# Performance work log

Measured on AMD Instinct MI355X. Metric: run time of the kernel, lower is better.

## Reference

```python
import jax, jax.numpy as jnp
from jax import lax
from jax.scipy.special import logsumexp
import numpy as np

N_NODES = 6144
N_EDGES = 98304
N_FEAT = 128
N_TPLT = 16
M_NODES = 10
N_CG = 5        # conditional-gradient (Frank-Wolfe) outer iterations
N_SINK = 50     # log-domain Sinkhorn iterations for the linearized OT subproblem


def setup_inputs() -> dict:
    key = jax.random.key(0)
    k1, k2, k3, k4 = jax.random.split(key, 4)
    x = jax.random.normal(k1, (N_NODES, N_FEAT), dtype=jnp.float32)
    edge_index = jax.random.randint(k2, (2, N_EDGES), 0, N_NODES, dtype=jnp.int64)
    # template_initialisation: uniform(0,1) adjacencies, symmetrized; normal features; zero q0/alpha0
    t_raw = jax.random.uniform(k3, (N_TPLT, M_NODES, M_NODES), dtype=jnp.float32)
    templates = 0.5 * (t_raw + jnp.transpose(t_raw, (0, 2, 1)))
    templates_features = jax.random.normal(k4, (N_TPLT, M_NODES, N_FEAT), dtype=jnp.float32)
    q0 = jnp.zeros((N_TPLT, M_NODES), dtype=jnp.float32)
    alpha0 = jnp.zeros((1,), dtype=jnp.float32)
    return {"x": x, "edge_index": edge_index, "templates": templates,
            "templates_features": templates_features, "q0": q0, "alpha0": alpha0}


def _sinkhorn_log(G, logp, logq, reg):
    """Log-domain Sinkhorn solving min <G,T> + reg*H(T) over U(p,q)."""
    K = -G / reg                         # [n, m]
    f0 = jnp.zeros_like(logp)

    def body(f, _):
        g = logq - logsumexp(K + f[:, None], axis=0)
        f = logp - logsumexp(K + g[None, :], axis=1)
        return f, None

    f, _ = lax.scan(body, f0, None, length=N_SINK)
    g = logq - logsumexp(K + f[:, None], axis=0)
    return jnp.exp(f[:, None] + K + g[None, :])


def _fgw2(M, C1, C2, p, q, alpha):
    """Fused Gromov-Wasserstein distance (square loss) via conditional gradient.
    M: [n,m] feature cost, C1: [n,n] graph structure, C2: [m,m] template structure."""
    # init_matrix (square loss): constC = f1(C1) p 1^T + 1 q^T f2(C2)^T
    constC = (C1 ** 2 @ p)[:, None] + (C2 ** 2 @ q)[None, :]   # [n, m]
    logp, logq = jnp.log(p), jnp.log(q)
    T0 = p[:, None] * q[None, :]

    def step(T, _):
        C1TC2 = C1 @ T @ C2                                   # [n, m] (dominant cost)
        grad = (1.0 - alpha) * M + alpha * 2.0 * (constC - 2.0 * C1TC2)
        reg = lax.stop_gradient(0.05 * jnp.max(jnp.abs(grad)) + 1e-8)
        Tn = _sinkhorn_log(grad, logp, logq, reg)             # linearized OT subproblem
        dT = Tn - T
        # exact line search for the quadratic objective along dT
        C1dTC2 = C1 @ dT @ C2
        a = -2.0 * alpha * jnp.sum(C1dTC2 * dT)
        b = (1.0 - alpha) * jnp.sum(M * dT) + alpha * (jnp.sum(constC * dT) - 4.0 * jnp.sum(C1TC2 * dT))
        tau = jnp.where(a > 0.0,
                        jnp.clip(-b / (2.0 * a + 1e-16), 0.0, 1.0),
                        jnp.where(a + b < 0.0, 1.0, 0.0))
        return T + tau * dT, None

    T, _ = lax.scan(step, T0, None, length=N_CG)
    gw = jnp.sum((constC - 2.0 * (C1 @ T @ C2)) * T)
    wass = jnp.sum(M * T)
    return (1.0 - alpha) * wass + alpha * gw


def reference(x, edge_index, templates, templates_features, q0, alpha0):
    alpha = jax.nn.sigmoid(alpha0)[0]
    q = jax.nn.softmax(q0, axis=1)                            # [T, m] template node weights
    n = x.shape[0]
    # dense adjacency from edge list (symmetrized)
    A = jnp.zeros((n, n), dtype=x.dtype).at[edge_index[0], edge_index[1]].set(1.0)
    C1 = jnp.maximum(A, A.T)                                  # [n, n]
    p = jnp.full((n,), 1.0 / n, dtype=x.dtype)
    # squared euclidean feature cost per template: [T, n, m]
    M = (jnp.sum(x ** 2, axis=1)[None, :, None]
         + jnp.sum(templates_features ** 2, axis=-1)[:, None, :]
         - 2.0 * jnp.einsum('nf,tmf->tnm', x, templates_features))
    dists = jax.vmap(_fgw2, in_axes=(0, None, 0, None, 0, None))(M, C1, templates, p, q, alpha)
    return dists                                              # [n_templates]
```

## Files before the change

### kernel.cpp

```cpp
#include <hip/hip_runtime.h>
#include <hip/hip_cooperative_groups.h>

namespace cgx = cooperative_groups;

static constexpr int NN  = 6144;
static constexpr int NE  = 98304;
static constexpr int NF  = 128;
static constexpr int NT  = 16;
static constexpr int MN  = 10;
static constexpr int NCG = 5;
static constexpr int NSK = 50;
static constexpr int WPR = NN / 32;
static constexpr int TPB = 768;
static constexpr int NBLK = 256;
static constexpr int RPT = NN / TPB;
static constexpr int NW  = TPB / 64;

static_assert(TPB * RPT == NN, "row mapping");

static constexpr size_t OFF_M   = 0;
static constexpr size_t OFF_T4  = OFF_M  + (size_t)NT * NN * MN;
static constexpr size_t OFF_T1  = OFF_T4 + (size_t)NT * NN * 4;
static constexpr size_t OFF_C4  = OFF_T1 + (size_t)NT * NN;
static constexpr size_t OFF_C1  = OFF_C4 + (size_t)NT * NN * 4;
static constexpr size_t OFF_D4  = OFF_C1 + (size_t)NT * NN;
static constexpr size_t OFF_D1  = OFF_D4 + (size_t)NT * NN * 4;
static constexpr size_t OFF_RS  = OFF_D1 + (size_t)NT * NN;
static constexpr size_t OFF_DEG = OFF_RS + NN;
static constexpr size_t OFF_CI  = OFF_DEG + NN;
static constexpr size_t OFF_NNZ = OFF_CI + NE;

static constexpr int LDS_PL  = NN * 20;
static constexpr int LDS_SP  = TPB * 7 * 4;
static constexpr int LDS_DYN = LDS_PL + LDS_SP;

__device__ __forceinline__ unsigned f2bf(float f) {
    unsigned u = __float_as_uint(f);
    return (u + 0x7fffu + ((u >> 16) & 1u)) >> 16;
}
__device__ __forceinline__ unsigned packbf(float a, float b) { return f2bf(a) | (f2bf(b) << 16); }
__device__ __forceinline__ float bflo(unsigned w) { return __uint_as_float(w << 16); }
__device__ __forceinline__ float bfhi(unsigned w) { return __uint_as_float(w & 0xffff0000u); }

extern __shared__ char sMem[];

__global__ __launch_bounds__(TPB) void tfgw_kernel(
    const float* __restrict__ x, const void* __restrict__ eiv,
    const float* __restrict__ tpl, const float* __restrict__ tf,
    const float* __restrict__ q0, const float* __restrict__ a0,
    float* __restrict__ out, float* __restrict__ W)
{
    __shared__ float sC2[MN * MN];
    __shared__ float sq[MN], scq[MN], sqC2[MN], sNSQ[MN];
    __shared__ unsigned svp[5];
    __shared__ unsigned svP2[5];
    __shared__ float sCv[5];
    __shared__ float sRed[3 * NW];
    __shared__ float sBC[2];
    __shared__ float sDots[4];

    const int tid = threadIdx.x;
    const int bid = blockIdx.x;

    unsigned* BM    = (unsigned*)(W + OFF_T4);
    int* rowst      = (int*)(W + OFF_RS);
    int* degi       = (int*)(W + OFF_DEG);
    unsigned short* colix = (unsigned short*)(W + OFF_CI);
    int* nnzc       = (int*)(W + OFF_NNZ);
    float* Mw  = W + OFF_M;

    uint4*    PL4x = (uint4*)sMem;
    unsigned* PL1x = (unsigned*)(sMem + NN * 16);
    unsigned* sPp  = (unsigned*)(sMem + LDS_PL);

    const float alpha  = 1.f / (1.f + __expf(-a0[0]));
    const float invn   = 1.f / (float)NN;
    const float alpha2 = 2.f * alpha;
    const float oma    = 1.f - alpha;

    cgx::grid_group grid = cgx::this_grid();

    for (int idx = bid * TPB + tid; idx < NN * WPR; idx += NBLK * TPB) BM[idx] = 0u;
    if (bid == 0 && tid == 0) *nnzc = 0;
    grid.sync();

    {
        const unsigned* uw = (const unsigned*)eiv;
        const bool is64 = (uw[1] == 0u && uw[3] == 0u && uw[5] == 0u);
        for (int e = bid * TPB + tid; e < NE; e += NBLK * TPB) {
            int s, d;
            if (is64) {
                s = (int)((const long long*)eiv)[e];
                d = (int)((const long long*)eiv)[NE + e];
            } else {
                s = ((const int*)eiv)[e];
                d = ((const int*)eiv)[NE + e];
            }
            atomicOr(&BM[(size_t)s * WPR + (d >> 5)], 1u << (d & 31));
            atomicOr(&BM[(size_t)d * WPR + (s >> 5)], 1u << (s & 31));
        }
        float* sTF = (float*)sMem;
        const int t = bid >> 4, rb = bid & 15;
        for (int k = tid; k < MN * NF; k += TPB) sTF[k] = tf[t * MN * NF + k];
        __syncthreads();
        if (tid < MN) {
            float s = 0.f;
            for (int k = 0; k < NF; ++k) { float v = sTF[tid * NF + k]; s += v * v; }
            sNSQ[tid] = s;
        }
        __syncthreads();
        if (tid < 384) {
            const int i = rb * 384 + tid;
            const float4* x4 = (const float4*)(x + (size_t)i * NF);
            const float4* t4 = (const float4*)sTF;
            float acc[MN]; float xn = 0.f;
            #pragma unroll
            for (int j = 0; j < MN; ++j) acc[j] = 0.f;
            for (int k4 = 0; k4 < NF / 4; ++k4) {
                float4 xv = x4[k4];
                xn += xv.x * xv.x + xv.y * xv.y + xv.z * xv.z + xv.w * xv.w;
                #pragma unroll
                for (int j = 0; j < MN; ++j) {
                    float4 tv = t4[j * (NF / 4) + k4];
                    acc[j] += xv.x * tv.x + xv.y * tv.y + xv.z * tv.z + xv.w * tv.w;
                }
            }
            float* Mrow = Mw + (size_t)t * NN * MN + (size_t)i * MN;
            #pragma unroll
            for (int j = 0; j < MN; ++j) Mrow[j] = xn + sNSQ[j] - 2.f * acc[j];
        }
    }
    grid.sync();

    {
        const int i = bid * TPB + tid;
        if (i < NN) {
            int cnt = 0;
            for (int w = 0; w < WPR; ++w) cnt += __popc(BM[(size_t)i * WPR + w]);
            int st = atomicAdd(nnzc, cnt);
            rowst[i] = st; degi[i] = cnt;
            int p = st;
            for (int w = 0; w < WPR; ++w) {
                unsigned m = BM[(size_t)i * WPR + w];
                while (m) { int b = __ffs(m) - 1; m &= m - 1; colix[p++] = (unsigned short)((w << 5) + b); }
            }
        }
    }
    grid.sync();

    if (bid >= NT) return;

    const int t = bid;
    float* Mb = Mw + (size_t)t * NN * MN;
    uint4*    Tb4 = (uint4*)(W + OFF_T4) + (size_t)t * NN;
    unsigned* Tb1 = (unsigned*)(W + OFF_T1) + (size_t)t * NN;
    uint4*    Cb4 = (uint4*)(W + OFF_C4) + (size_t)t * NN;
    unsigned* Cb1 = (unsigned*)(W + OFF_C1) + (size_t)t * NN;
    uint4*    Db4 = (uint4*)(W + OFF_D4) + (size_t)t * NN;
    unsigned* Db1 = (unsigned*)(W + OFF_D1) + (size_t)t * NN;

    if (tid == 0) {
        float qv[MN]; float qm = -1e30f;
        for (int j = 0; j < MN; ++j) { qv[j] = q0[t * MN + j]; qm = fmaxf(qm, qv[j]); }
        float qs = 0.f;
        for (int j = 0; j < MN; ++j) { qv[j] = __expf(qv[j] - qm); qs += qv[j]; }
        for (int j = 0; j < MN; ++j) { qv[j] /= qs; sq[j] = qv[j]; }
        for (int j = 0; j < MN; ++j) {
            float s2 = 0.f, s1 = 0.f;
            for (int k = 0; k < MN; ++k) {
                float cjk = tpl[t * MN * MN + j * MN + k];
                s2 += cjk * cjk * qv[k];
                s1 += tpl[t * MN * MN + k * MN + j] * qv[k];
            }
            scq[j] = s2; sqC2[j] = s1;
        }
    }
    for (int k = tid; k < MN * MN; k += TPB) sC2[k] = tpl[t * MN * MN + k];
    __syncthreads();

    for (int cgi = 0; cgi < NCG; ++cgi) {
        if (tid == 0) {
            float tau = 0.f;
            if (cgi > 0) {
                float a = -2.f * alpha * sDots[3];
                float b = oma * sDots[0] + alpha * (sDots[1] - 4.f * sDots[2]);
                if (a > 0.f) tau = fminf(fmaxf(-b / (2.f * a + 1e-16f), 0.f), 1.f);
                else         tau = (a + b < 0.f) ? 1.f : 0.f;
            }
            sBC[0] = tau;
        }
        if (tid < 5) svP2[tid] = 0xFFFFFFFFu;
        __syncthreads();
        const float tau = sBC[0];
        if (cgi > 0 && tau == 0.f) break;

        float gmax = 0.f;
        #pragma unroll
        for (int k = 0; k < RPT; ++k) {
            const int r = tid + k * TPB;
            const float cp = (float)degi[r] * invn;
            float C[MN];
            if (cgi == 0) {
                uint4 tw4; unsigned tw1;
                uint4 cw4; unsigned cw1;
                tw4.x = packbf(sq[0]*invn, sq[1]*invn); tw4.y = packbf(sq[2]*invn, sq[3]*invn);
                tw4.z = packbf(sq[4]*invn, sq[5]*invn); tw4.w = packbf(sq[6]*invn, sq[7]*invn);
                tw1   = packbf(sq[8]*invn, sq[9]*invn);
                cw4.x = packbf(cp*sqC2[0], cp*sqC2[1]); cw4.y = packbf(cp*sqC2[2], cp*sqC2[3]);
                cw4.z = packbf(cp*sqC2[4], cp*sqC2[5]); cw4.w = packbf(cp*sqC2[6], cp*sqC2[7]);
                cw1   = packbf(cp*sqC2[8], cp*sqC2[9]);
                Tb4[r] = tw4; Tb1[r] = tw1; Cb4[r] = cw4; Cb1[r] = cw1;
                C[0]=bflo(cw4.x); C[1]=bfhi(cw4.x); C[2]=bflo(cw4.y); C[3]=bfhi(cw4.y);
                C[4]=bflo(cw4.z); C[5]=bfhi(cw4.z); C[6]=bflo(cw4.w); C[7]=bfhi(cw4.w);
                C[8]=bflo(cw1);   C[9]=bfhi(cw1);
            } else {
                float dd[MN];
                uint4 a = PL4x[r]; unsigned b4 = PL1x[r];
                dd[0]=bflo(a.x); dd[1]=bfhi(a.x); dd[2]=bflo(a.y); dd[3]=bfhi(a.y);
                dd[4]=bflo(a.z); dd[5]=bfhi(a.z); dd[6]=bflo(a.w); dd[7]=bfhi(a.w);
                dd[8]=bflo(b4);  dd[9]=bfhi(b4);
                uint4 tw4 = Tb4[r]; unsigned tw1 = Tb1[r];
                uint4 cw4 = Cb4[r]; unsigned cw1 = Cb1[r];
                uint4 Dw4 = Db4[r]; unsigned Dw1 = Db1[r];
                float T[MN], Dd[MN];
                T[0]=bflo(tw4.x); T[1]=bfhi(tw4.x); T[2]=bflo(tw4.y); T[3]=bfhi(tw4.y);
                T[4]=bflo(tw4.z); T[5]=bfhi(tw4.z); T[6]=bflo(tw4.w); T[7]=bfhi(tw4.w);
                T[8]=bflo(tw1);   T[9]=bfhi(tw1);
                C[0]=bflo(cw4.x); C[1]=bfhi(cw4.x); C[2]=bflo(cw4.y); C[3]=bfhi(cw4.y);
                C[4]=bflo(cw4.z); C[5]=bfhi(cw4.z); C[6]=bflo(cw4.w); C[7]=bfhi(cw4.w);
                C[8]=bflo(cw1);   C[9]=bfhi(cw1);
                Dd[0]=bflo(Dw4.x); Dd[1]=bfhi(Dw4.x); Dd[2]=bflo(Dw4.y); Dd[3]=bfhi(Dw4.y);
                Dd[4]=bflo(Dw4.z); Dd[5]=bfhi(Dw4.z); Dd[6]=bflo(Dw4.w); Dd[7]=bfhi(Dw4.w);
                Dd[8]=bflo(Dw1);   Dd[9]=bfhi(Dw1);
                #pragma unroll
                for (int j = 0; j < MN; ++j) { T[j] += tau * dd[j]; C[j] += tau * Dd[j]; }
                uint4 ntw4; unsigned ntw1; uint4 ncw4; unsigned ncw1;
                ntw4.x = packbf(T[0],T[1]); ntw4.y = packbf(T[2],T[3]);
                ntw4.z = packbf(T[4],T[5]); ntw4.w = packbf(T[6],T[7]);
                ntw1   = packbf(T[8],T[9]);
                ncw4.x = packbf(C[0],C[1]); ncw4.y = packbf(C[2],C[3]);
                ncw4.z = packbf(C[4],C[5]); ncw4.w = packbf(C[6],C[7]);
                ncw1   = packbf(C[8],C[9]);
                Tb4[r] = ntw4; Tb1[r] = ntw1; Cb4[r] = ncw4; Cb1[r] = ncw1;
                C[0]=bflo(ncw4.x); C[1]=bfhi(ncw4.x); C[2]=bflo(ncw4.y); C[3]=bfhi(ncw4.y);
                C[4]=bflo(ncw4.z); C[5]=bfhi(ncw4.z); C[6]=bflo(ncw4.w); C[7]=bfhi(ncw4.w);
                C[8]=bflo(ncw1);   C[9]=bfhi(ncw1);
            }
            float g[MN];
            #pragma unroll
            for (int h = 0; h < 5; ++h) {
                float2 mv = *(const float2*)(Mb + (size_t)r * MN + 2*h);
                g[2*h]   = oma * mv.x + alpha2 * (cp + scq[2*h]   - 2.f * C[2*h]);
                g[2*h+1] = oma * mv.y + alpha2 * (cp + scq[2*h+1] - 2.f * C[2*h+1]);
                gmax = fmaxf(gmax, fmaxf(__builtin_fabsf(g[2*h]), __builtin_fabsf(g[2*h+1])));
            }
            PL4x[r] = make_uint4(packbf(g[0],g[1]), packbf(g[2],g[3]),
                                 packbf(g[4],g[5]), packbf(g[6],g[7]));
            PL1x[r] = packbf(g[8], g[9]);
        }
        #pragma unroll
        for (int d = 32; d; d >>= 1) gmax = fmaxf(gmax, __shfl_xor(gmax, d));
        if ((tid & 63) == 0) sRed[tid >> 6] = gmax;
        __syncthreads();
        if (tid == 0) {
            float m = sRed[0];
            for (int w = 1; w < NW; ++w) m = fmaxf(m, sRed[w]);
            sBC[1] = 1.f / (0.05f * m + 1e-8f);
        }
        __syncthreads();
        const float invreg = sBC[1];

        #pragma unroll
        for (int k = 0; k < RPT; ++k) {
            const int r = tid + k * TPB;
            uint4 a = PL4x[r]; unsigned b4 = PL1x[r];
            float g[MN];
            g[0]=bflo(a.x); g[1]=bfhi(a.x); g[2]=bflo(a.y); g[3]=bfhi(a.y);
            g[4]=bflo(a.z); g[5]=bfhi(a.z); g[6]=bflo(a.w); g[7]=bfhi(a.w);
            g[8]=bflo(b4);  g[9]=bfhi(b4);
            float e[MN];
            #pragma unroll
            for (int j = 0; j < MN; ++j) e[j] = __expf(-g[j] * invreg);
            PL4x[r] = make_uint4(packbf(e[0],e[1]), packbf(e[2],e[3]),
                                 packbf(e[4],e[5]), packbf(e[6],e[7]));
            PL1x[r] = packbf(e[8], e[9]);
        }

        if (cgi == 0) {
            float a[MN];
            #pragma unroll
            for (int j = 0; j < MN; ++j) a[j] = 0.f;
            #pragma unroll
            for (int k = 0; k < RPT; ++k) {
                const int r = tid + k * TPB;
                uint4 q = PL4x[r]; unsigned b4 = PL1x[r];
                a[0]+=bflo(q.x); a[1]+=bfhi(q.x); a[2]+=bflo(q.y); a[3]+=bfhi(q.y);
                a[4]+=bflo(q.z); a[5]+=bfhi(q.z); a[6]+=bflo(q.w); a[7]+=bfhi(q.w);
                a[8]+=bflo(b4);  a[9]+=bfhi(b4);
            }
            #pragma unroll
            for (int p = 0; p < 5; ++p) sPp[tid * 7 + p] = packbf(a[2*p], a[2*p+1]);
            __syncthreads();
            if (tid < 320) {
                const int p = tid >> 6, c = tid & 63;
                float s0 = 0.f, s1 = 0.f;
                #pragma unroll
                for (int kk = 0; kk < NW; ++kk) {
                    unsigned w = sPp[(c + (kk << 6)) * 7 + p];
                    s0 += bflo(w); s1 += bfhi(w);
                }
                #pragma unroll
                for (int d = 32; d; d >>= 1) { s0 += __shfl_xor(s0, d); s1 += __shfl_xor(s1, d); }
                if (c == 0) svp[p] = packbf(sq[2*p] / s0, sq[2*p+1] / s1);
            }
            __syncthreads();
        }

        for (int it = 1; it <= NSK; ++it) {
            float vv[MN];
            #pragma unroll
            for (int p = 0; p < 5; ++p) {
                unsigned w = svp[p];
                vv[2*p] = bflo(w); vv[2*p+1] = bfhi(w);
            }
            float a[MN];
            #pragma unroll
            for (int j = 0; j < MN; ++j) a[j] = 0.f;
            #pragma unroll
            for (int k = 0; k < RPT; ++k) {
                const int r = tid + k * TPB;
                uint4 q = PL4x[r]; unsigned b4 = PL1x[r];
                float e[MN];
                e[0]=bflo(q.x); e[1]=bfhi(q.x); e[2]=bflo(q.y); e[3]=bfhi(q.y);
                e[4]=bflo(q.z); e[5]=bfhi(q.z); e[6]=bflo(q.w); e[7]=bfhi(q.w);
                e[8]=bflo(b4);  e[9]=bfhi(b4);
                float R = 0.f;
                #pragma unroll
                for (int j = 0; j < MN; ++j) R += e[j] * vv[j];
                const float u = invn * __builtin_amdgcn_rcpf(R);
                #pragma unroll
                for (int j = 0; j < MN; ++j) a[j] += e[j] * u;
            }
            #pragma unroll
            for (int p = 0; p < 5; ++p) sPp[tid * 7 + p] = packbf(a[2*p], a[2*p+1]);
            __syncthreads();
            if (tid < 320) {
                const int p = tid >> 6, c = tid & 63;
                float s0 = 0.f, s1 = 0.f;
                #pragma unroll
                for (int kk = 0; kk < NW; ++kk) {
                    unsigned w = sPp[(c + (kk << 6)) * 7 + p];
                    s0 += bflo(w); s1 += bfhi(w);
                }
                #pragma unroll
                for (int d = 32; d; d >>= 1) { s0 += __shfl_xor(s0, d); s1 += __shfl_xor(s1, d); }
                if (c == 0) {
                    unsigned pw = packbf(sq[2*p] / s0, sq[2*p+1] / s1);
                    unsigned old = svp[p], old2 = svP2[p];
                    sCv[p] = (pw == old || pw == old2) ? 1.f : 0.f;
                    svP2[p] = old;
                    svp[p] = pw;
                }
            }
            __syncthreads();
            if (sCv[0] + sCv[1] + sCv[2] + sCv[3] + sCv[4] == 5.f) break;
        }

        {
            float vv[MN];
            #pragma unroll
            for (int p = 0; p < 5; ++p) {
                unsigned w = svp[p];
                vv[2*p] = bflo(w); vv[2*p+1] = bfhi(w);
            }
            float sMdT = 0.f, sCdT = 0.f, sCTdT = 0.f;
            #pragma unroll
            for (int k = 0; k < RPT; ++k) {
                const int r = tid + k * TPB;
                const float cp = (float)degi[r] * invn;
                uint4 q = PL4x[r]; unsigned b4 = PL1x[r];
                float e[MN], dd[MN];
                e[0]=bflo(q.x); e[1]=bfhi(q.x); e[2]=bflo(q.y); e[3]=bfhi(q.y);
                e[4]=bflo(q.z); e[5]=bfhi(q.z); e[6]=bflo(q.w); e[7]=bfhi(q.w);
                e[8]=bflo(b4);  e[9]=bfhi(b4);
                float R = 0.f;
                #pragma unroll
                for (int j = 0; j < MN; ++j) R += e[j] * vv[j];
                const float u = invn * __builtin_amdgcn_rcpf(R);
                uint4 tw4 = Tb4[r]; unsigned tw1 = Tb1[r];
                uint4 cw4 = Cb4[r]; unsigned cw1 = Cb1[r];
                float T[MN], C[MN];
                T[0]=bflo(tw4.x); T[1]=bfhi(tw4.x); T[2]=bflo(tw4.y); T[3]=bfhi(tw4.y);
                T[4]=bflo(tw4.z); T[5]=bfhi(tw4.z); T[6]=bflo(tw4.w); T[7]=bfhi(tw4.w);
                T[8]=bflo(tw1);   T[9]=bfhi(tw1);
                C[0]=bflo(cw4.x); C[1]=bfhi(cw4.x); C[2]=bflo(cw4.y); C[3]=bfhi(cw4.y);
                C[4]=bflo(cw4.z); C[5]=bfhi(cw4.z); C[6]=bflo(cw4.w); C[7]=bfhi(cw4.w);
                C[8]=bflo(cw1);   C[9]=bfhi(cw1);
                #pragma unroll
                for (int h = 0; h < 5; ++h) {
                    float2 mv = *(const float2*)(Mb + (size_t)r * MN + 2*h);
                    float d0 = u * e[2*h]   * vv[2*h]   - T[2*h];
                    float d1 = u * e[2*h+1] * vv[2*h+1] - T[2*h+1];
                    dd[2*h] = d0; dd[2*h+1] = d1;
                    sMdT  += mv.x * d0 + mv.y * d1;
                    sCdT  += (cp + scq[2*h]) * d0 + (cp + scq[2*h+1]) * d1;
                    sCTdT += C[2*h] * d0 + C[2*h+1] * d1;
                }
                PL4x[r] = make_uint4(packbf(dd[0],dd[1]), packbf(dd[2],dd[3]),
                                     packbf(dd[4],dd[5]), packbf(dd[6],dd[7]));
                PL1x[r] = packbf(dd[8], dd[9]);
            }
            #pragma unroll
            for (int d = 32; d; d >>= 1) {
                sMdT  += __shfl_xor(sMdT, d);
                sCdT  += __shfl_xor(sCdT, d);
                sCTdT += __shfl_xor(sCTdT, d);
            }
            if ((tid & 63) == 0) {
                const int w = tid >> 6;
                sRed[w] = sMdT; sRed[NW + w] = sCdT; sRed[2*NW + w] = sCTdT;
            }
            __syncthreads();
            if (tid == 0) {
                float r0 = 0.f, r1 = 0.f, r2 = 0.f;
                for (int w = 0; w < NW; ++w) { r0 += sRed[w]; r1 += sRed[NW+w]; r2 += sRed[2*NW+w]; }
                sDots[0] = r0; sDots[1] = r1; sDots[2] = r2;
            }
        }

        {
            float dot = 0.f;
            #pragma unroll
            for (int k = 0; k < RPT; ++k) {
                const int r = tid + k * TPB;
                float y[MN];
                #pragma unroll
                for (int j = 0; j < MN; ++j) y[j] = 0.f;
                const int st = rowst[r], dg = degi[r];
                const unsigned short* cl = colix + st;
                for (int e = 0; e < dg; ++e) {
                    const int j = cl[e];
                    uint4 q = PL4x[j]; unsigned b4 = PL1x[j];
                    y[0] += bflo(q.x); y[1] += bfhi(q.x);
                    y[2] += bflo(q.y); y[3] += bfhi(q.y);
                    y[4] += bflo(q.z); y[5] += bfhi(q.z);
                    y[6] += bflo(q.w); y[7] += bfhi(q.w);
                    y[8] += bflo(b4);  y[9] += bfhi(b4);
                }
                uint4 q = PL4x[r]; unsigned b4 = PL1x[r];
                float dd[MN];
                dd[0]=bflo(q.x); dd[1]=bfhi(q.x); dd[2]=bflo(q.y); dd[3]=bfhi(q.y);
                dd[4]=bflo(q.z); dd[5]=bfhi(q.z); dd[6]=bflo(q.w); dd[7]=bfhi(q.w);
                dd[8]=bflo(b4);  dd[9]=bfhi(b4);
                float o[MN];
                #pragma unroll
                for (int h = 0; h < 5; ++h) {
                    float o0 = 0.f, o1 = 0.f;
                    #pragma unroll
                    for (int j = 0; j < MN; ++j) {
                        o0 += y[j] * sC2[j * MN + 2*h];
                        o1 += y[j] * sC2[j * MN + 2*h + 1];
                    }
                    o[2*h] = o0; o[2*h+1] = o1;
                    dot += o0 * dd[2*h] + o1 * dd[2*h+1];
                }
                Db4[r] = make_uint4(packbf(o[0],o[1]), packbf(o[2],o[3]),
                                    packbf(o[4],o[5]), packbf(o[6],o[7]));
                Db1[r] = packbf(o[8], o[9]);
            }
            #pragma unroll
            for (int d = 32; d; d >>= 1) dot += __shfl_xor(dot, d);
            if ((tid & 63) == 0) sRed[tid >> 6] = dot;
            __syncthreads();
            if (tid == 0) {
                float s = 0.f;
                for (int w = 0; w < NW; ++w) s += sRed[w];
                sDots[3] = s;
            }
            __syncthreads();
        }
    }

    if (tid == 0) {
        float a = -2.f * alpha * sDots[3];
        float b = oma * sDots[0] + alpha * (sDots[1] - 4.f * sDots[2]);
        float tau;
        if (a > 0.f) tau = fminf(fmaxf(-b / (2.f * a + 1e-16f), 0.f), 1.f);
        else         tau = (a + b < 0.f) ? 1.f : 0.f;
        sBC[0] = tau;
    }
    __syncthreads();
    {
        const float tau = sBC[0];
        float gw = 0.f, wass = 0.f;
        #pragma unroll
        for (int k = 0; k < RPT; ++k) {
            const int r = tid + k * TPB;
            const float cp = (float)degi[r] * invn;
            uint4 q = PL4x[r]; unsigned b4 = PL1x[r];
            float dd[MN];
            dd[0]=bflo(q.x); dd[1]=bfhi(q.x); dd[2]=bflo(q.y); dd[3]=bfhi(q.y);
            dd[4]=bflo(q.z); dd[5]=bfhi(q.z); dd[6]=bflo(q.w); dd[7]=bfhi(q.w);
            dd[8]=bflo(b4);  dd[9]=bfhi(b4);
            uint4 tw4 = Tb4[r]; unsigned tw1 = Tb1[r];
            uint4 cw4 = Cb4[r]; unsigned cw1 = Cb1[r];
            uint4 Dw4 = Db4[r]; unsigned Dw1 = Db1[r];
            float T[MN], C[MN], Dd[MN];
            T[0]=bflo(tw4.x); T[1]=bfhi(tw4.x); T[2]=bflo(tw4.y); T[3]=bfhi(tw4.y);
            T[4]=bflo(tw4.z); T[5]=bfhi(tw4.z); T[6]=bflo(tw4.w); T[7]=bfhi(tw4.w);
            T[8]=bflo(tw1);   T[9]=bfhi(tw1);
            C[0]=bflo(cw4.x); C[1]=bfhi(cw4.x); C[2]=bflo(cw4.y); C[3]=bfhi(cw4.y);
            C[4]=bflo(cw4.z); C[5]=bfhi(cw4.z); C[6]=bflo(cw4.w); C[7]=bfhi(cw4.w);
            C[8]=bflo(cw1);   C[9]=bfhi(cw1);
            Dd[0]=bflo(Dw4.x); Dd[1]=bfhi(Dw4.x); Dd[2]=bflo(Dw4.y); Dd[3]=bfhi(Dw4.y);
            Dd[4]=bflo(Dw4.z); Dd[5]=bfhi(Dw4.z); Dd[6]=bflo(Dw4.w); Dd[7]=bfhi(Dw4.w);
            Dd[8]=bflo(Dw1);   Dd[9]=bfhi(Dw1);
            #pragma unroll
            for (int h = 0; h < 5; ++h) {
                float2 mv = *(const float2*)(Mb + (size_t)r * MN + 2*h);
                float Tf0 = T[2*h]   + tau * dd[2*h];
                float Tf1 = T[2*h+1] + tau * dd[2*h+1];
                float Cf0 = C[2*h]   + tau * Dd[2*h];
                float Cf1 = C[2*h+1] + tau * Dd[2*h+1];
                gw   += (cp + scq[2*h]   - 2.f * Cf0) * Tf0
                      + (cp + scq[2*h+1] - 2.f * Cf1) * Tf1;
                wass += mv.x * Tf0 + mv.y * Tf1;
            }
        }
        #pragma unroll
        for (int d = 32; d; d >>= 1) {
            gw   += __shfl_xor(gw, d);
            wass += __shfl_xor(wass, d);
        }
        if ((tid & 63) == 0) { sRed[tid >> 6] = gw; sRed[NW + (tid >> 6)] = wass; }
        __syncthreads();
        if (tid == 0) {
            float g = 0.f, ws = 0.f;
            for (int w = 0; w < NW; ++w) { g += sRed[w]; ws += sRed[NW + w]; }
            out[t] = oma * ws + alpha * g;
        }
    }
}

extern "C" void kernel_launch(void* const* d_in, const int* in_sizes, int n_in,
                              void* d_out, int out_size, void* d_ws, size_t ws_size,
                              hipStream_t stream) {
    const float* x   = (const float*)d_in[0];
    const void*  ei  = d_in[1];
    const float* tpl = (const float*)d_in[2];
    const float* tfp = (const float*)d_in[3];
    const float* q0  = (const float*)d_in[4];
    const float* a0  = (const float*)d_in[5];
    float* outp = (float*)d_out;
    float* Wp   = (float*)d_ws;
    (void)hipFuncSetAttribute(reinterpret_cast<const void*>(&tfgw_kernel),
                              hipFuncAttributeMaxDynamicSharedMemorySize, LDS_DYN);
    void* args[] = { &x, &ei, &tpl, &tfp, &q0, &a0, &outp, &Wp };
    hipLaunchCooperativeKernel(reinterpret_cast<const void*>(&tfgw_kernel),
                               dim3(NBLK), dim3(TPB), args, LDS_DYN, stream);
}
```

Measured before the change: 713.1 us.

## Split each template's FGW solve across eight blocks with flag-based inter-block reductions

Each template was previously handled by one block, which looped over all 6144 rows. Now eight blocks share a template, and each thread owns one row with its Sinkhorn state held in registers. Per-iteration column sums, gradient maxima and line-search dot products are exchanged between the eight blocks through global memory slots tagged with sequence numbers, using release stores and acquire polls. This spreads the serial Sinkhorn and CG work over eight times as many CUs, at the cost of a global spin-wait round trip on every Sinkhorn iteration and extra global traffic for the direction matrix.

```diff
diff --git a/kernel.cpp b/kernel.cpp
--- a/kernel.cpp
+++ b/kernel.cpp
@@ -13,26 +13,28 @@
 static constexpr int WPR = NN / 32;
 static constexpr int TPB = 768;
 static constexpr int NBLK = 256;
-static constexpr int RPT = NN / TPB;
+static constexpr int G   = 8;
 static constexpr int NW  = TPB / 64;
 
-static_assert(TPB * RPT == NN, "row mapping");
+static_assert(G * TPB == NN, "row mapping");
 
 static constexpr size_t OFF_M   = 0;
-static constexpr size_t OFF_T4  = OFF_M  + (size_t)NT * NN * MN;
-static constexpr size_t OFF_T1  = OFF_T4 + (size_t)NT * NN * 4;
-static constexpr size_t OFF_C4  = OFF_T1 + (size_t)NT * NN;
-static constexpr size_t OFF_C1  = OFF_C4 + (size_t)NT * NN * 4;
-static constexpr size_t OFF_D4  = OFF_C1 + (size_t)NT * NN;
-static constexpr size_t OFF_D1  = OFF_D4 + (size_t)NT * NN * 4;
-static constexpr size_t OFF_RS  = OFF_D1 + (size_t)NT * NN;
-static constexpr size_t OFF_DEG = OFF_RS + NN;
+static constexpr size_t OFF_T4  = OFF_M   + (size_t)NT * NN * MN;
+static constexpr size_t OFF_T1  = OFF_T4  + (size_t)NT * NN * 4;
+static constexpr size_t OFF_C4  = OFF_T1  + (size_t)NT * NN;
+static constexpr size_t OFF_C1  = OFF_C4  + (size_t)NT * NN * 4;
+static constexpr size_t OFF_D4  = OFF_C1  + (size_t)NT * NN;
+static constexpr size_t OFF_D1  = OFF_D4  + (size_t)NT * NN * 4;
+static constexpr size_t OFF_DD4 = OFF_D1  + (size_t)NT * NN;
+static constexpr size_t OFF_DD1 = OFF_DD4 + (size_t)NT * NN * 4;
+static constexpr size_t OFF_RS  = OFF_DD1 + (size_t)NT * NN;
+static constexpr size_t OFF_DEG = OFF_RS  + NN;
 static constexpr size_t OFF_CI  = OFF_DEG + NN;
-static constexpr size_t OFF_NNZ = OFF_CI + NE;
-
-static constexpr int LDS_PL  = NN * 20;
+static constexpr size_t OFF_NNZ = OFF_CI  + NE;
+static constexpr size_t OFF_SL  = OFF_NNZ + 16;
+
 static constexpr int LDS_SP  = TPB * 7 * 4;
-static constexpr int LDS_DYN = LDS_PL + LDS_SP;
+static constexpr int LDS_DYN = 86016;
 
 __device__ __forceinline__ unsigned f2bf(float f) {
     unsigned u = __float_as_uint(f);
@@ -41,6 +43,20 @@
 __device__ __forceinline__ unsigned packbf(float a, float b) { return f2bf(a) | (f2bf(b) << 16); }
 __device__ __forceinline__ float bflo(unsigned w) { return __uint_as_float(w << 16); }
 __device__ __forceinline__ float bfhi(unsigned w) { return __uint_as_float(w & 0xffff0000u); }
+
+__device__ __forceinline__ void slput(unsigned long long* p, unsigned st, unsigned pay) {
+    __hip_atomic_store(p, ((unsigned long long)st << 32) | (unsigned long long)pay,
+                       __ATOMIC_RELEASE, __HIP_MEMORY_SCOPE_AGENT);
+}
+__device__ __forceinline__ unsigned slpoll(const unsigned long long* p, unsigned st) {
+    unsigned long long v;
+    do { v = __hip_atomic_load(p, __ATOMIC_ACQUIRE, __HIP_MEMORY_SCOPE_AGENT); }
+    while ((unsigned)(v >> 32) != st);
+    return (unsigned)v;
+}
+__device__ __forceinline__ unsigned slget(const unsigned long long* p) {
+    return (unsigned)__hip_atomic_load(p, __ATOMIC_RELAXED, __HIP_MEMORY_SCOPE_AGENT);
+}
 
 extern __shared__ char sMem[];
 
@@ -52,12 +68,9 @@
 {
     __shared__ float sC2[MN * MN];
     __shared__ float sq[MN], scq[MN], sqC2[MN], sNSQ[MN];
-    __shared__ unsigned svp[5];
-    __shared__ unsigned svP2[5];
-    __shared__ float sCv[5];
+    __shared__ __align__(16) float sv[12];
     __shared__ float sRed[3 * NW];
     __shared__ float sBC[2];
-    __shared__ float sDots[4];
 
     const int tid = threadIdx.x;
     const int bid = blockIdx.x;
@@ -68,10 +81,9 @@
     unsigned short* colix = (unsigned short*)(W + OFF_CI);
     int* nnzc       = (int*)(W + OFF_NNZ);
     float* Mw  = W + OFF_M;
-
-    uint4*    PL4x = (uint4*)sMem;
-    unsigned* PL1x = (unsigned*)(sMem + NN * 16);
-    unsigned* sPp  = (unsigned*)(sMem + LDS_PL);
+    unsigned long long* SL = (unsigned long long*)(W + OFF_SL);
+
+    unsigned* sPp = (unsigned*)sMem;
 
     const float alpha  = 1.f / (1.f + __expf(-a0[0]));
     const float invn   = 1.f / (float)NN;
@@ -81,6 +93,8 @@
     cgx::grid_group grid = cgx::this_grid();
 
     for (int idx = bid * TPB + tid; idx < NN * WPR; idx += NBLK * TPB) BM[idx] = 0u;
+    for (int idx = bid * TPB + tid; idx < NT * G * 8 * 2; idx += NBLK * TPB)
+        ((unsigned*)SL)[idx] = 0u;
     if (bid == 0 && tid == 0) *nnzc = 0;
     grid.sync();
 
@@ -100,8 +114,8 @@
             atomicOr(&BM[(size_t)d * WPR + (s >> 5)], 1u << (s & 31));
         }
         float* sTF = (float*)sMem;
-        const int t = bid >> 4, rb = bid & 15;
-        for (int k = tid; k < MN * NF; k += TPB) sTF[k] = tf[t * MN * NF + k];
+        const int tt = bid >> 4, rb = bid & 15;
+        for (int k = tid; k < MN * NF; k += TPB) sTF[k] = tf[tt * MN * NF + k];
         __syncthreads();
         if (tid < MN) {
             float s = 0.f;
@@ -125,7 +139,7 @@
                     acc[j] += xv.x * tv.x + xv.y * tv.y + xv.z * tv.z + xv.w * tv.w;
                 }
             }
-            float* Mrow = Mw + (size_t)t * NN * MN + (size_t)i * MN;
+            float* Mrow = Mw + (size_t)tt * NN * MN + (size_t)i * MN;
             #pragma unroll
             for (int j = 0; j < MN; ++j) Mrow[j] = xn + sNSQ[j] - 2.f * acc[j];
         }
@@ -137,9 +151,9 @@
         if (i < NN) {
             int cnt = 0;
             for (int w = 0; w < WPR; ++w) cnt += __popc(BM[(size_t)i * WPR + w]);
-            int st = atomicAdd(nnzc, cnt);
-            rowst[i] = st; degi[i] = cnt;
-            int p = st;
+            int st0 = atomicAdd(nnzc, cnt);
+            rowst[i] = st0; degi[i] = cnt;
+            int p = st0;
             for (int w = 0; w < WPR; ++w) {
                 unsigned m = BM[(size_t)i * WPR + w];
                 while (m) { int b = __ffs(m) - 1; m &= m - 1; colix[p++] = (unsigned short)((w << 5) + b); }
@@ -148,16 +162,23 @@
     }
     grid.sync();
 
-    if (bid >= NT) return;
-
-    const int t = bid;
-    float* Mb = Mw + (size_t)t * NN * MN;
+    if (bid >= NT * G) return;
+
+    const int t = bid & 15;
+    const int g = bid >> 4;
+    const int r = g * TPB + tid;
+    unsigned long long* SLt = SL + (size_t)t * G * 8;
+    unsigned long long* SLg = SLt + (size_t)g * 8;
+
     uint4*    Tb4 = (uint4*)(W + OFF_T4) + (size_t)t * NN;
     unsigned* Tb1 = (unsigned*)(W + OFF_T1) + (size_t)t * NN;
     uint4*    Cb4 = (uint4*)(W + OFF_C4) + (size_t)t * NN;
     unsigned* Cb1 = (unsigned*)(W + OFF_C1) + (size_t)t * NN;
     uint4*    Db4 = (uint4*)(W + OFF_D4) + (size_t)t * NN;
     unsigned* Db1 = (unsigned*)(W + OFF_D1) + (size_t)t * NN;
+    uint4*    DD4 = (uint4*)(W + OFF_DD4) + (size_t)t * NN;
+    unsigned* DD1 = (unsigned*)(W + OFF_DD1) + (size_t)t * NN;
+    const float* Mb = Mw + (size_t)t * NN * MN;
 
     if (tid == 0) {
         float qv[MN]; float qm = -1e30f;
@@ -178,31 +199,75 @@
     for (int k = tid; k < MN * MN; k += TPB) sC2[k] = tpl[t * MN * MN + k];
     __syncthreads();
 
+    const float cp = (float)degi[r] * invn;
+    const int rst = rowst[r], rdg = degi[r];
+
+    unsigned st = 0;
+    float e[MN];
+    float dd[MN];
+    #pragma unroll
+    for (int j = 0; j < MN; ++j) { e[j] = 0.f; dd[j] = 0.f; }
+
+    auto sink_round = [&](const float* a) {
+        #pragma unroll
+        for (int p = 0; p < 5; ++p) sPp[tid * 7 + p] = packbf(a[2*p], a[2*p+1]);
+        __syncthreads();
+        float s0 = 0.f, s1 = 0.f;
+        if (tid < 320) {
+            const int p = tid >> 6, c = tid & 63;
+            #pragma unroll
+            for (int kk = 0; kk < NW; ++kk) {
+                unsigned w = sPp[(c + (kk << 6)) * 7 + p];
+                s0 += bflo(w); s1 += bfhi(w);
+            }
+            #pragma unroll
+            for (int d = 32; d; d >>= 1) { s0 += __shfl_xor(s0, d); s1 += __shfl_xor(s1, d); }
+        }
+        ++st;
+        if (tid < 320 && (tid & 63) == 0) slput(SLg + (tid >> 6), st, packbf(s0, s1));
+        if (tid < 40) {
+            const int pp = tid >> 3, gg = tid & 7;
+            unsigned pay = slpoll(SLt + gg * 8 + pp, st);
+            float f0 = bflo(pay), f1 = bfhi(pay);
+            f0 += __shfl_xor(f0, 1); f0 += __shfl_xor(f0, 2); f0 += __shfl_xor(f0, 4);
+            f1 += __shfl_xor(f1, 1); f1 += __shfl_xor(f1, 2); f1 += __shfl_xor(f1, 4);
+            if (gg == 0) { sv[2*pp] = sq[2*pp] / f0; sv[2*pp+1] = sq[2*pp+1] / f1; }
+        }
+        __syncthreads();
+    };
+
     for (int cgi = 0; cgi < NCG; ++cgi) {
-        if (tid == 0) {
-            float tau = 0.f;
-            if (cgi > 0) {
-                float a = -2.f * alpha * sDots[3];
-                float b = oma * sDots[0] + alpha * (sDots[1] - 4.f * sDots[2]);
-                if (a > 0.f) tau = fminf(fmaxf(-b / (2.f * a + 1e-16f), 0.f), 1.f);
-                else         tau = (a + b < 0.f) ? 1.f : 0.f;
-            }
-            sBC[0] = tau;
-        }
-        if (tid < 5) svP2[tid] = 0xFFFFFFFFu;
-        __syncthreads();
-        const float tau = sBC[0];
-        if (cgi > 0 && tau == 0.f) break;
-
-        float gmax = 0.f;
-        #pragma unroll
-        for (int k = 0; k < RPT; ++k) {
-            const int r = tid + k * TPB;
-            const float cp = (float)degi[r] * invn;
+        float tau = 0.f;
+        if (cgi > 0) {
+            if (tid < G) {
+                float a3 = __uint_as_float(slpoll(SLt + tid * 8 + 3, st));
+                float a0v = __uint_as_float(slget(SLt + tid * 8 + 0));
+                float a1v = __uint_as_float(slget(SLt + tid * 8 + 1));
+                float a2v = __uint_as_float(slget(SLt + tid * 8 + 2));
+                #pragma unroll
+                for (int d = 1; d < 8; d <<= 1) {
+                    a0v += __shfl_xor(a0v, d); a1v += __shfl_xor(a1v, d);
+                    a2v += __shfl_xor(a2v, d); a3  += __shfl_xor(a3, d);
+                }
+                if (tid == 0) {
+                    float aq = -2.f * alpha * a3;
+                    float bq = oma * a0v + alpha * (a1v - 4.f * a2v);
+                    float tv;
+                    if (aq > 0.f) tv = fminf(fmaxf(-bq / (2.f * aq + 1e-16f), 0.f), 1.f);
+                    else          tv = (aq + bq < 0.f) ? 1.f : 0.f;
+                    sBC[0] = tv;
+                }
+            }
+            __syncthreads();
+            tau = sBC[0];
+            if (tau == 0.f) break;
+        }
+
+        float graw[MN];
+        {
             float C[MN];
             if (cgi == 0) {
-                uint4 tw4; unsigned tw1;
-                uint4 cw4; unsigned cw1;
+                uint4 tw4; unsigned tw1; uint4 cw4; unsigned cw1;
                 tw4.x = packbf(sq[0]*invn, sq[1]*invn); tw4.y = packbf(sq[2]*invn, sq[3]*invn);
                 tw4.z = packbf(sq[4]*invn, sq[5]*invn); tw4.w = packbf(sq[6]*invn, sq[7]*invn);
                 tw1   = packbf(sq[8]*invn, sq[9]*invn);
@@ -214,11 +279,6 @@
                 C[4]=bflo(cw4.z); C[5]=bfhi(cw4.z); C[6]=bflo(cw4.w); C[7]=bfhi(cw4.w);
                 C[8]=bflo(cw1);   C[9]=bfhi(cw1);
             } else {
-                float dd[MN];
-                uint4 a = PL4x[r]; unsigned b4 = PL1x[r];
-                dd[0]=bflo(a.x); dd[1]=bfhi(a.x); dd[2]=bflo(a.y); dd[3]=bfhi(a.y);
-                dd[4]=bflo(a.z); dd[5]=bfhi(a.z); dd[6]=bflo(a.w); dd[7]=bfhi(a.w);
-                dd[8]=bflo(b4);  dd[9]=bfhi(b4);
                 uint4 tw4 = Tb4[r]; unsigned tw1 = Tb1[r];
                 uint4 cw4 = Cb4[r]; unsigned cw1 = Cb1[r];
                 uint4 Dw4 = Db4[r]; unsigned Dw1 = Db1[r];
@@ -234,298 +294,219 @@
                 Dd[8]=bflo(Dw1);   Dd[9]=bfhi(Dw1);
                 #pragma unroll
                 for (int j = 0; j < MN; ++j) { T[j] += tau * dd[j]; C[j] += tau * Dd[j]; }
-                uint4 ntw4; unsigned ntw1; uint4 ncw4; unsigned ncw1;
-                ntw4.x = packbf(T[0],T[1]); ntw4.y = packbf(T[2],T[3]);
-                ntw4.z = packbf(T[4],T[5]); ntw4.w = packbf(T[6],T[7]);
-                ntw1   = packbf(T[8],T[9]);
-                ncw4.x = packbf(C[0],C[1]); ncw4.y = packbf(C[2],C[3]);
-                ncw4.z = packbf(C[4],C[5]); ncw4.w = packbf(C[6],C[7]);
-                ncw1   = packbf(C[8],C[9]);
-                Tb4[r] = ntw4; Tb1[r] = ntw1; Cb4[r] = ncw4; Cb1[r] = ncw1;
-                C[0]=bflo(ncw4.x); C[1]=bfhi(ncw4.x); C[2]=bflo(ncw4.y); C[3]=bfhi(ncw4.y);
-                C[4]=bflo(ncw4.z); C[5]=bfhi(ncw4.z); C[6]=bflo(ncw4.w); C[7]=bfhi(ncw4.w);
-                C[8]=bflo(ncw1);   C[9]=bfhi(ncw1);
-            }
-            float g[MN];
+                uint4 n4; unsigned n1;
+                n4.x = packbf(T[0],T[1]); n4.y = packbf(T[2],T[3]);
+                n4.z = packbf(T[4],T[5]); n4.w = packbf(T[6],T[7]); n1 = packbf(T[8],T[9]);
+                Tb4[r] = n4; Tb1[r] = n1;
+                n4.x = packbf(C[0],C[1]); n4.y = packbf(C[2],C[3]);
+                n4.z = packbf(C[4],C[5]); n4.w = packbf(C[6],C[7]); n1 = packbf(C[8],C[9]);
+                Cb4[r] = n4; Cb1[r] = n1;
+                C[0]=bflo(n4.x); C[1]=bfhi(n4.x); C[2]=bflo(n4.y); C[3]=bfhi(n4.y);
+                C[4]=bflo(n4.z); C[5]=bfhi(n4.z); C[6]=bflo(n4.w); C[7]=bfhi(n4.w);
+                C[8]=bflo(n1);   C[9]=bfhi(n1);
+            }
+            float gmax = 0.f;
             #pragma unroll
             for (int h = 0; h < 5; ++h) {
                 float2 mv = *(const float2*)(Mb + (size_t)r * MN + 2*h);
-                g[2*h]   = oma * mv.x + alpha2 * (cp + scq[2*h]   - 2.f * C[2*h]);
-                g[2*h+1] = oma * mv.y + alpha2 * (cp + scq[2*h+1] - 2.f * C[2*h+1]);
-                gmax = fmaxf(gmax, fmaxf(__builtin_fabsf(g[2*h]), __builtin_fabsf(g[2*h+1])));
-            }
-            PL4x[r] = make_uint4(packbf(g[0],g[1]), packbf(g[2],g[3]),
-                                 packbf(g[4],g[5]), packbf(g[6],g[7]));
-            PL1x[r] = packbf(g[8], g[9]);
-        }
+                graw[2*h]   = oma * mv.x + alpha2 * (cp + scq[2*h]   - 2.f * C[2*h]);
+                graw[2*h+1] = oma * mv.y + alpha2 * (cp + scq[2*h+1] - 2.f * C[2*h+1]);
+                gmax = fmaxf(gmax, fmaxf(__builtin_fabsf(graw[2*h]), __builtin_fabsf(graw[2*h+1])));
+            }
+            #pragma unroll
+            for (int d = 32; d; d >>= 1) gmax = fmaxf(gmax, __shfl_xor(gmax, d));
+            if ((tid & 63) == 0) sRed[tid >> 6] = gmax;
+            __syncthreads();
+            ++st;
+            if (tid == 0) {
+                float m = sRed[0];
+                for (int w = 1; w < NW; ++w) m = fmaxf(m, sRed[w]);
+                slput(SLg + 6, st, __float_as_uint(m));
+            }
+            if (tid < G) {
+                float mg = __uint_as_float(slpoll(SLt + tid * 8 + 6, st));
+                mg = fmaxf(mg, __shfl_xor(mg, 1));
+                mg = fmaxf(mg, __shfl_xor(mg, 2));
+                mg = fmaxf(mg, __shfl_xor(mg, 4));
+                if (tid == 0) sBC[1] = 1.f / (0.05f * mg + 1e-8f);
+            }
+            __syncthreads();
+        }
+        const float invreg = sBC[1];
         #pragma unroll
-        for (int d = 32; d; d >>= 1) gmax = fmaxf(gmax, __shfl_xor(gmax, d));
-        if ((tid & 63) == 0) sRed[tid >> 6] = gmax;
-        __syncthreads();
-        if (tid == 0) {
-            float m = sRed[0];
-            for (int w = 1; w < NW; ++w) m = fmaxf(m, sRed[w]);
-            sBC[1] = 1.f / (0.05f * m + 1e-8f);
-        }
-        __syncthreads();
-        const float invreg = sBC[1];
-
-        #pragma unroll
-        for (int k = 0; k < RPT; ++k) {
-            const int r = tid + k * TPB;
-            uint4 a = PL4x[r]; unsigned b4 = PL1x[r];
-            float g[MN];
-            g[0]=bflo(a.x); g[1]=bfhi(a.x); g[2]=bflo(a.y); g[3]=bfhi(a.y);
-            g[4]=bflo(a.z); g[5]=bfhi(a.z); g[6]=bflo(a.w); g[7]=bfhi(a.w);
-            g[8]=bflo(b4);  g[9]=bfhi(b4);
-            float e[MN];
-            #pragma unroll
-            for (int j = 0; j < MN; ++j) e[j] = __expf(-g[j] * invreg);
-            PL4x[r] = make_uint4(packbf(e[0],e[1]), packbf(e[2],e[3]),
-                                 packbf(e[4],e[5]), packbf(e[6],e[7]));
-            PL1x[r] = packbf(e[8], e[9]);
-        }
-
-        if (cgi == 0) {
+        for (int j = 0; j < MN; ++j) e[j] = __expf(-graw[j] * invreg);
+
+        if (cgi == 0) sink_round(e);
+        for (int it = 0; it < NSK; ++it) {
+            float vv[MN];
+            {
+                const float4* s4 = (const float4*)sv;
+                float4 v0 = s4[0], v1 = s4[1]; float2 v2 = *(const float2*)(sv + 8);
+                vv[0]=v0.x; vv[1]=v0.y; vv[2]=v0.z; vv[3]=v0.w;
+                vv[4]=v1.x; vv[5]=v1.y; vv[6]=v1.z; vv[7]=v1.w;
+                vv[8]=v2.x; vv[9]=v2.y;
+            }
+            float R = 0.f;
+            #pragma unroll
+            for (int j = 0; j < MN; ++j) R += e[j] * vv[j];
+            const float u = invn * __builtin_amdgcn_rcpf(R);
             float a[MN];
             #pragma unroll
-            for (int j = 0; j < MN; ++j) a[j] = 0.f;
-            #pragma unroll
-            for (int k = 0; k < RPT; ++k) {
-                const int r = tid + k * TPB;
-                uint4 q = PL4x[r]; unsigned b4 = PL1x[r];
-                a[0]+=bflo(q.x); a[1]+=bfhi(q.x); a[2]+=bflo(q.y); a[3]+=bfhi(q.y);
-                a[4]+=bflo(q.z); a[5]+=bfhi(q.z); a[6]+=bflo(q.w); a[7]+=bfhi(q.w);
-                a[8]+=bflo(b4);  a[9]+=bfhi(b4);
-            }
-            #pragma unroll
-            for (int p = 0; p < 5; ++p) sPp[tid * 7 + p] = packbf(a[2*p], a[2*p+1]);
-            __syncthreads();
-            if (tid < 320) {
-                const int p = tid >> 6, c = tid & 63;
-                float s0 = 0.f, s1 = 0.f;
-                #pragma unroll
-                for (int kk = 0; kk < NW; ++kk) {
-                    unsigned w = sPp[(c + (kk << 6)) * 7 + p];
-                    s0 += bflo(w); s1 += bfhi(w);
-                }
-                #pragma unroll
-                for (int d = 32; d; d >>= 1) { s0 += __shfl_xor(s0, d); s1 += __shfl_xor(s1, d); }
-                if (c == 0) svp[p] = packbf(sq[2*p] / s0, sq[2*p+1] / s1);
-            }
-            __syncthreads();
-        }
-
-        for (int it = 1; it <= NSK; ++it) {
-            float vv[MN];
-            #pragma unroll
-            for (int p = 0; p < 5; ++p) {
-                unsigned w = svp[p];
-                vv[2*p] = bflo(w); vv[2*p+1] = bfhi(w);
-            }
-            float a[MN];
-            #pragma unroll
-            for (int j = 0; j < MN; ++j) a[j] = 0.f;
-            #pragma unroll
-            for (int k = 0; k < RPT; ++k) {
-                const int r = tid + k * TPB;
-                uint4 q = PL4x[r]; unsigned b4 = PL1x[r];
-                float e[MN];
-                e[0]=bflo(q.x); e[1]=bfhi(q.x); e[2]=bflo(q.y); e[3]=bfhi(q.y);
-                e[4]=bflo(q.z); e[5]=bfhi(q.z); e[6]=bflo(q.w); e[7]=bfhi(q.w);
-                e[8]=bflo(b4);  e[9]=bfhi(b4);
-                float R = 0.f;
-                #pragma unroll
-                for (int j = 0; j < MN; ++j) R += e[j] * vv[j];
-                const float u = invn * __builtin_amdgcn_rcpf(R);
-                #pragma unroll
-                for (int j = 0; j < MN; ++j) a[j] += e[j] * u;
-            }
-            #pragma unroll
-            for (int p = 0; p < 5; ++p) sPp[tid * 7 + p] = packbf(a[2*p], a[2*p+1]);
-            __syncthreads();
-            if (tid < 320) {
-                const int p = tid >> 6, c = tid & 63;
-                float s0 = 0.f, s1 = 0.f;
-                #pragma unroll
-                for (int kk = 0; kk < NW; ++kk) {
-                    unsigned w = sPp[(c + (kk << 6)) * 7 + p];
-                    s0 += bflo(w); s1 += bfhi(w);
-                }
-                #pragma unroll
-                for (int d = 32; d; d >>= 1) { s0 += __shfl_xor(s0, d); s1 += __shfl_xor(s1, d); }
-                if (c == 0) {
-                    unsigned pw = packbf(sq[2*p] / s0, sq[2*p+1] / s1);
-                    unsigned old = svp[p], old2 = svP2[p];
-                    sCv[p] = (pw == old || pw == old2) ? 1.f : 0.f;
-                    svP2[p] = old;
-                    svp[p] = pw;
-                }
-            }
-            __syncthreads();
-            if (sCv[0] + sCv[1] + sCv[2] + sCv[3] + sCv[4] == 5.f) break;
+            for (int j = 0; j < MN; ++j) a[j] = e[j] * u;
+            sink_round(a);
         }
 
         {
             float vv[MN];
-            #pragma unroll
-            for (int p = 0; p < 5; ++p) {
-                unsigned w = svp[p];
-                vv[2*p] = bflo(w); vv[2*p+1] = bfhi(w);
-            }
-            float sMdT = 0.f, sCdT = 0.f, sCTdT = 0.f;
-            #pragma unroll
-            for (int k = 0; k < RPT; ++k) {
-                const int r = tid + k * TPB;
-                const float cp = (float)degi[r] * invn;
-                uint4 q = PL4x[r]; unsigned b4 = PL1x[r];
-                float e[MN], dd[MN];
-                e[0]=bflo(q.x); e[1]=bfhi(q.x); e[2]=bflo(q.y); e[3]=bfhi(q.y);
-                e[4]=bflo(q.z); e[5]=bfhi(q.z); e[6]=bflo(q.w); e[7]=bfhi(q.w);
-                e[8]=bflo(b4);  e[9]=bfhi(b4);
-                float R = 0.f;
-                #pragma unroll
-                for (int j = 0; j < MN; ++j) R += e[j] * vv[j];
-                const float u = invn * __builtin_amdgcn_rcpf(R);
-                uint4 tw4 = Tb4[r]; unsigned tw1 = Tb1[r];
-                uint4 cw4 = Cb4[r]; unsigned cw1 = Cb1[r];
-                float T[MN], C[MN];
-                T[0]=bflo(tw4.x); T[1]=bfhi(tw4.x); T[2]=bflo(tw4.y); T[3]=bfhi(tw4.y);
-                T[4]=bflo(tw4.z); T[5]=bfhi(tw4.z); T[6]=bflo(tw4.w); T[7]=bfhi(tw4.w);
-                T[8]=bflo(tw1);   T[9]=bfhi(tw1);
-                C[0]=bflo(cw4.x); C[1]=bfhi(cw4.x); C[2]=bflo(cw4.y); C[3]=bfhi(cw4.y);
-                C[4]=bflo(cw4.z); C[5]=bfhi(cw4.z); C[6]=bflo(cw4.w); C[7]=bfhi(cw4.w);
-                C[8]=bflo(cw1);   C[9]=bfhi(cw1);
-                #pragma unroll
-                for (int h = 0; h < 5; ++h) {
-                    float2 mv = *(const float2*)(Mb + (size_t)r * MN + 2*h);
-                    float d0 = u * e[2*h]   * vv[2*h]   - T[2*h];
-                    float d1 = u * e[2*h+1] * vv[2*h+1] - T[2*h+1];
-                    dd[2*h] = d0; dd[2*h+1] = d1;
-                    sMdT  += mv.x * d0 + mv.y * d1;
-                    sCdT  += (cp + scq[2*h]) * d0 + (cp + scq[2*h+1]) * d1;
-                    sCTdT += C[2*h] * d0 + C[2*h+1] * d1;
-                }
-                PL4x[r] = make_uint4(packbf(dd[0],dd[1]), packbf(dd[2],dd[3]),
-                                     packbf(dd[4],dd[5]), packbf(dd[6],dd[7]));
-                PL1x[r] = packbf(dd[8], dd[9]);
-            }
-            #pragma unroll
-            for (int d = 32; d; d >>= 1) {
-                sMdT  += __shfl_xor(sMdT, d);
-                sCdT  += __shfl_xor(sCdT, d);
-                sCTdT += __shfl_xor(sCTdT, d);
-            }
-            if ((tid & 63) == 0) {
-                const int w = tid >> 6;
-                sRed[w] = sMdT; sRed[NW + w] = sCdT; sRed[2*NW + w] = sCTdT;
-            }
-            __syncthreads();
-            if (tid == 0) {
-                float r0 = 0.f, r1 = 0.f, r2 = 0.f;
-                for (int w = 0; w < NW; ++w) { r0 += sRed[w]; r1 += sRed[NW+w]; r2 += sRed[2*NW+w]; }
-                sDots[0] = r0; sDots[1] = r1; sDots[2] = r2;
-            }
-        }
-
-        {
-            float dot = 0.f;
-            #pragma unroll
-            for (int k = 0; k < RPT; ++k) {
-                const int r = tid + k * TPB;
-                float y[MN];
-                #pragma unroll
-                for (int j = 0; j < MN; ++j) y[j] = 0.f;
-                const int st = rowst[r], dg = degi[r];
-                const unsigned short* cl = colix + st;
-                for (int e = 0; e < dg; ++e) {
-                    const int j = cl[e];
-                    uint4 q = PL4x[j]; unsigned b4 = PL1x[j];
-                    y[0] += bflo(q.x); y[1] += bfhi(q.x);
-                    y[2] += bflo(q.y); y[3] += bfhi(q.y);
-                    y[4] += bflo(q.z); y[5] += bfhi(q.z);
-                    y[6] += bflo(q.w); y[7] += bfhi(q.w);
-                    y[8] += bflo(b4);  y[9] += bfhi(b4);
-                }
-                uint4 q = PL4x[r]; unsigned b4 = PL1x[r];
-                float dd[MN];
-                dd[0]=bflo(q.x); dd[1]=bfhi(q.x); dd[2]=bflo(q.y); dd[3]=bfhi(q.y);
-                dd[4]=bflo(q.z); dd[5]=bfhi(q.z); dd[6]=bflo(q.w); dd[7]=bfhi(q.w);
-                dd[8]=bflo(b4);  dd[9]=bfhi(b4);
-                float o[MN];
-                #pragma unroll
-                for (int h = 0; h < 5; ++h) {
-                    float o0 = 0.f, o1 = 0.f;
-                    #pragma unroll
-                    for (int j = 0; j < MN; ++j) {
-                        o0 += y[j] * sC2[j * MN + 2*h];
-                        o1 += y[j] * sC2[j * MN + 2*h + 1];
-                    }
-                    o[2*h] = o0; o[2*h+1] = o1;
-                    dot += o0 * dd[2*h] + o1 * dd[2*h+1];
-                }
-                Db4[r] = make_uint4(packbf(o[0],o[1]), packbf(o[2],o[3]),
-                                    packbf(o[4],o[5]), packbf(o[6],o[7]));
-                Db1[r] = packbf(o[8], o[9]);
-            }
-            #pragma unroll
-            for (int d = 32; d; d >>= 1) dot += __shfl_xor(dot, d);
-            if ((tid & 63) == 0) sRed[tid >> 6] = dot;
-            __syncthreads();
-            if (tid == 0) {
-                float s = 0.f;
-                for (int w = 0; w < NW; ++w) s += sRed[w];
-                sDots[3] = s;
-            }
-            __syncthreads();
-        }
-    }
-
-    if (tid == 0) {
-        float a = -2.f * alpha * sDots[3];
-        float b = oma * sDots[0] + alpha * (sDots[1] - 4.f * sDots[2]);
-        float tau;
-        if (a > 0.f) tau = fminf(fmaxf(-b / (2.f * a + 1e-16f), 0.f), 1.f);
-        else         tau = (a + b < 0.f) ? 1.f : 0.f;
-        sBC[0] = tau;
-    }
-    __syncthreads();
-    {
-        const float tau = sBC[0];
-        float gw = 0.f, wass = 0.f;
-        #pragma unroll
-        for (int k = 0; k < RPT; ++k) {
-            const int r = tid + k * TPB;
-            const float cp = (float)degi[r] * invn;
-            uint4 q = PL4x[r]; unsigned b4 = PL1x[r];
-            float dd[MN];
-            dd[0]=bflo(q.x); dd[1]=bfhi(q.x); dd[2]=bflo(q.y); dd[3]=bfhi(q.y);
-            dd[4]=bflo(q.z); dd[5]=bfhi(q.z); dd[6]=bflo(q.w); dd[7]=bfhi(q.w);
-            dd[8]=bflo(b4);  dd[9]=bfhi(b4);
+            {
+                const float4* s4 = (const float4*)sv;
+                float4 v0 = s4[0], v1 = s4[1]; float2 v2 = *(const float2*)(sv + 8);
+                vv[0]=v0.x; vv[1]=v0.y; vv[2]=v0.z; vv[3]=v0.w;
+                vv[4]=v1.x; vv[5]=v1.y; vv[6]=v1.z; vv[7]=v1.w;
+                vv[8]=v2.x; vv[9]=v2.y;
+            }
+            float R = 0.f;
+            #pragma unroll
+            for (int j = 0; j < MN; ++j) R += e[j] * vv[j];
+            const float u = invn * __builtin_amdgcn_rcpf(R);
             uint4 tw4 = Tb4[r]; unsigned tw1 = Tb1[r];
             uint4 cw4 = Cb4[r]; unsigned cw1 = Cb1[r];
-            uint4 Dw4 = Db4[r]; unsigned Dw1 = Db1[r];
-            float T[MN], C[MN], Dd[MN];
+            float T[MN], C[MN];
             T[0]=bflo(tw4.x); T[1]=bfhi(tw4.x); T[2]=bflo(tw4.y); T[3]=bfhi(tw4.y);
             T[4]=bflo(tw4.z); T[5]=bfhi(tw4.z); T[6]=bflo(tw4.w); T[7]=bfhi(tw4.w);
             T[8]=bflo(tw1);   T[9]=bfhi(tw1);
             C[0]=bflo(cw4.x); C[1]=bfhi(cw4.x); C[2]=bflo(cw4.y); C[3]=bfhi(cw4.y);
             C[4]=bflo(cw4.z); C[5]=bfhi(cw4.z); C[6]=bflo(cw4.w); C[7]=bfhi(cw4.w);
             C[8]=bflo(cw1);   C[9]=bfhi(cw1);
-            Dd[0]=bflo(Dw4.x); Dd[1]=bfhi(Dw4.x); Dd[2]=bflo(Dw4.y); Dd[3]=bfhi(Dw4.y);
-            Dd[4]=bflo(Dw4.z); Dd[5]=bfhi(Dw4.z); Dd[6]=bflo(Dw4.w); Dd[7]=bfhi(Dw4.w);
-            Dd[8]=bflo(Dw1);   Dd[9]=bfhi(Dw1);
+            float sMdT = 0.f, sCdT = 0.f, sCTdT = 0.f;
             #pragma unroll
             for (int h = 0; h < 5; ++h) {
                 float2 mv = *(const float2*)(Mb + (size_t)r * MN + 2*h);
-                float Tf0 = T[2*h]   + tau * dd[2*h];
-                float Tf1 = T[2*h+1] + tau * dd[2*h+1];
-                float Cf0 = C[2*h]   + tau * Dd[2*h];
-                float Cf1 = C[2*h+1] + tau * Dd[2*h+1];
-                gw   += (cp + scq[2*h]   - 2.f * Cf0) * Tf0
-                      + (cp + scq[2*h+1] - 2.f * Cf1) * Tf1;
-                wass += mv.x * Tf0 + mv.y * Tf1;
-            }
+                float d0 = u * e[2*h]   * vv[2*h]   - T[2*h];
+                float d1 = u * e[2*h+1] * vv[2*h+1] - T[2*h+1];
+                dd[2*h] = d0; dd[2*h+1] = d1;
+                sMdT  += mv.x * d0 + mv.y * d1;
+                sCdT  += (cp + scq[2*h]) * d0 + (cp + scq[2*h+1]) * d1;
+                sCTdT += C[2*h] * d0 + C[2*h+1] * d1;
+            }
+            DD4[r] = make_uint4(packbf(dd[0],dd[1]), packbf(dd[2],dd[3]),
+                                packbf(dd[4],dd[5]), packbf(dd[6],dd[7]));
+            DD1[r] = packbf(dd[8], dd[9]);
+            #pragma unroll
+            for (int d = 32; d; d >>= 1) {
+                sMdT  += __shfl_xor(sMdT, d);
+                sCdT  += __shfl_xor(sCdT, d);
+                sCTdT += __shfl_xor(sCTdT, d);
+            }
+            if ((tid & 63) == 0) {
+                const int w = tid >> 6;
+                sRed[w] = sMdT; sRed[NW + w] = sCdT; sRed[2*NW + w] = sCTdT;
+            }
+            __syncthreads();
+            ++st;
+            if (tid == 0) {
+                float r0 = 0.f, r1 = 0.f, r2 = 0.f;
+                for (int w = 0; w < NW; ++w) { r0 += sRed[w]; r1 += sRed[NW+w]; r2 += sRed[2*NW+w]; }
+                __threadfence();
+                slput(SLg + 0, st, __float_as_uint(r0));
+                slput(SLg + 1, st, __float_as_uint(r1));
+                slput(SLg + 2, st, __float_as_uint(r2));
+                slput(SLg + 7, st, 0u);
+            }
+            if (tid < G) (void)slpoll(SLt + tid * 8 + 7, st);
+            __syncthreads();
+            if (tid == 0) __threadfence();
+            __syncthreads();
+        }
+
+        {
+            float y[MN];
+            #pragma unroll
+            for (int j = 0; j < MN; ++j) y[j] = 0.f;
+            const unsigned short* cl = colix + rst;
+            for (int e2 = 0; e2 < rdg; ++e2) {
+                const int j = cl[e2];
+                uint4 q = DD4[j]; unsigned b4 = DD1[j];
+                y[0] += bflo(q.x); y[1] += bfhi(q.x);
+                y[2] += bflo(q.y); y[3] += bfhi(q.y);
+                y[4] += bflo(q.z); y[5] += bfhi(q.z);
+                y[6] += bflo(q.w); y[7] += bfhi(q.w);
+                y[8] += bflo(b4);  y[9] += bfhi(b4);
+            }
+            float o[MN]; float dot = 0.f;
+            #pragma unroll
+            for (int h = 0; h < 5; ++h) {
+                float o0 = 0.f, o1 = 0.f;
+                #pragma unroll
+                for (int j = 0; j < MN; ++j) {
+                    o0 += y[j] * sC2[j * MN + 2*h];
+                    o1 += y[j] * sC2[j * MN + 2*h + 1];
+                }
+                o[2*h] = o0; o[2*h+1] = o1;
+                dot += o0 * dd[2*h] + o1 * dd[2*h+1];
+            }
+            Db4[r] = make_uint4(packbf(o[0],o[1]), packbf(o[2],o[3]),
+                                packbf(o[4],o[5]), packbf(o[6],o[7]));
+            Db1[r] = packbf(o[8], o[9]);
+            #pragma unroll
+            for (int d = 32; d; d >>= 1) dot += __shfl_xor(dot, d);
+            if ((tid & 63) == 0) sRed[tid >> 6] = dot;
+            __syncthreads();
+            ++st;
+            if (tid == 0) {
+                float s = 0.f;
+                for (int w = 0; w < NW; ++w) s += sRed[w];
+                slput(SLg + 3, st, __float_as_uint(s));
+            }
+        }
+    }
+
+    {
+        if (tid < G) {
+            float a3 = __uint_as_float(slpoll(SLt + tid * 8 + 3, st));
+            float a0v = __uint_as_float(slget(SLt + tid * 8 + 0));
+            float a1v = __uint_as_float(slget(SLt + tid * 8 + 1));
+            float a2v = __uint_as_float(slget(SLt + tid * 8 + 2));
+            #pragma unroll
+            for (int d = 1; d < 8; d <<= 1) {
+                a0v += __shfl_xor(a0v, d); a1v += __shfl_xor(a1v, d);
+                a2v += __shfl_xor(a2v, d); a3  += __shfl_xor(a3, d);
+            }
+            if (tid == 0) {
+                float aq = -2.f * alpha * a3;
+                float bq = oma * a0v + alpha * (a1v - 4.f * a2v);
+                float tv;
+                if (aq > 0.f) tv = fminf(fmaxf(-bq / (2.f * aq + 1e-16f), 0.f), 1.f);
+                else          tv = (aq + bq < 0.f) ? 1.f : 0.f;
+                sBC[0] = tv;
+            }
+        }
+        __syncthreads();
+        const float tau = sBC[0];
+        uint4 tw4 = Tb4[r]; unsigned tw1 = Tb1[r];
+        uint4 cw4 = Cb4[r]; unsigned cw1 = Cb1[r];
+        uint4 Dw4 = Db4[r]; unsigned Dw1 = Db1[r];
+        float T[MN], C[MN], Dd[MN];
+        T[0]=bflo(tw4.x); T[1]=bfhi(tw4.x); T[2]=bflo(tw4.y); T[3]=bfhi(tw4.y);
+        T[4]=bflo(tw4.z); T[5]=bfhi(tw4.z); T[6]=bflo(tw4.w); T[7]=bfhi(tw4.w);
+        T[8]=bflo(tw1);   T[9]=bfhi(tw1);
+        C[0]=bflo(cw4.x); C[1]=bfhi(cw4.x); C[2]=bflo(cw4.y); C[3]=bfhi(cw4.y);
+        C[4]=bflo(cw4.z); C[5]=bfhi(cw4.z); C[6]=bflo(cw4.w); C[7]=bfhi(cw4.w);
+        C[8]=bflo(cw1);   C[9]=bfhi(cw1);
+        Dd[0]=bflo(Dw4.x); Dd[1]=bfhi(Dw4.x); Dd[2]=bflo(Dw4.y); Dd[3]=bfhi(Dw4.y);
+        Dd[4]=bflo(Dw4.z); Dd[5]=bfhi(Dw4.z); Dd[6]=bflo(Dw4.w); Dd[7]=bfhi(Dw4.w);
+        Dd[8]=bflo(Dw1);   Dd[9]=bfhi(Dw1);
+        float gw = 0.f, wass = 0.f;
+        #pragma unroll
+        for (int h = 0; h < 5; ++h) {
+            float2 mv = *(const float2*)(Mb + (size_t)r * MN + 2*h);
+            float Tf0 = T[2*h]   + tau * dd[2*h];
+            float Tf1 = T[2*h+1] + tau * dd[2*h+1];
+            float Cf0 = C[2*h]   + tau * Dd[2*h];
+            float Cf1 = C[2*h+1] + tau * Dd[2*h+1];
+            gw   += (cp + scq[2*h]   - 2.f * Cf0) * Tf0
+                  + (cp + scq[2*h+1] - 2.f * Cf1) * Tf1;
+            wass += mv.x * Tf0 + mv.y * Tf1;
         }
         #pragma unroll
         for (int d = 32; d; d >>= 1) {
@@ -534,10 +515,24 @@
         }
         if ((tid & 63) == 0) { sRed[tid >> 6] = gw; sRed[NW + (tid >> 6)] = wass; }
         __syncthreads();
+        ++st;
         if (tid == 0) {
-            float g = 0.f, ws = 0.f;
-            for (int w = 0; w < NW; ++w) { g += sRed[w]; ws += sRed[NW + w]; }
-            out[t] = oma * ws + alpha * g;
+            float sgw = 0.f, sws = 0.f;
+            for (int w = 0; w < NW; ++w) { sgw += sRed[w]; sws += sRed[NW + w]; }
+            slput(SLg + 4, st, __float_as_uint(sgw));
+            slput(SLg + 5, st, __float_as_uint(sws));
+        }
+        if (g == 0) {
+            if (tid < 16) {
+                const int gg = tid & 7, which = tid >> 3;
+                float val = __uint_as_float(slpoll(SLt + gg * 8 + 4 + which, st));
+                val += __shfl_xor(val, 1);
+                val += __shfl_xor(val, 2);
+                val += __shfl_xor(val, 4);
+                if (gg == 0) sRed[which] = val;
+            }
+            __syncthreads();
+            if (tid == 0) out[t] = oma * sRed[1] + alpha * sRed[0];
         }
     }
 }
```

After: 2.713 ms. +280.4%, slower.
